# Optimization experiments

Hardware: AMD Instinct MI355X
Metric: run time of the kernel (lower is better)

## Reference

```python
import jax, jax.numpy as jnp
import numpy as np

B, T, F_IN, N, H = 16, 2048, 64, 24, 64  # batch, time, input_dim, num_nodes, hidden_dim
ALPHA = 0.2        # LeakyReLU negative slope
NEG_INF = -9e15    # mask value used by the torch module


def setup_inputs() -> dict:
    key = jax.random.key(0)
    k0, k1, k2, k3, k4 = jax.random.split(key, 5)
    x = jax.random.normal(k0, (B, T, F_IN), dtype=jnp.float32)
    adj = jax.random.randint(k1, (N, N), 0, 2, dtype=jnp.int32)  # binary adjacency
    # input_projector: Linear(input_dim, num_nodes*hidden_dim)
    Wp = jax.random.normal(k2, (F_IN, N * H), dtype=jnp.float32) * 0.05
    bp = jnp.zeros((N * H,), dtype=jnp.float32)
    # GraphAttentionLayer params: W (in=H, out=H), a (2H, 1)
    W = jax.random.normal(k3, (H, H), dtype=jnp.float32) * 0.05
    a = jax.random.normal(k4, (2 * H, 1), dtype=jnp.float32) * 0.05
    return {"x": x, "adj": adj, "Wp": Wp, "bp": bp, "W": W, "a": a}


def reference(x, adj, Wp, bp, W, a):
    Bx, Tx, Fx = x.shape
    BT = Bx * Tx
    # input projector -> per-node features (BT, N, H)
    h = (x.reshape(BT, Fx) @ Wp + bp).reshape(BT, N, H)
    # GAT layer (concat=True), eval mode so dropout is identity
    Wh = h @ W  # (BT, N, H)
    # e[b,i,j] = LeakyReLU([Wh_i ; Wh_j] @ a) = LeakyReLU(Wh_i@a1 + Wh_j@a2)
    a1, a2 = a[:H, 0], a[H:, 0]
    f1 = Wh @ a1  # (BT, N)
    f2 = Wh @ a2  # (BT, N)
    e = f1[:, :, None] + f2[:, None, :]
    e = jnp.where(e > 0, e, ALPHA * e)
    e = jnp.where(adj[None, :, :] > 0, e, jnp.float32(NEG_INF))
    attn = jax.nn.softmax(e, axis=2)  # (BT, N, N)
    h_prime = jnp.einsum('bij,bjh->bih', attn, Wh)  # (BT, N, H)
    h_prime = jax.nn.elu(h_prime)
    out = h_prime.mean(axis=1)  # mean over nodes -> (BT, H)
    return out.reshape(Bx, Tx, H)
```

## Files before the change

kernel.cpp:

```cpp
#include <hip/hip_runtime.h>
#include <hip/hip_bf16.h>

#define F_IN   64
#define NN     24
#define HH     64
#define CC     1536
#define CCX    1584
#define NTILE  99
#define ROWS   16
#define BT_TOT (16 * 2048)
#define ALPHA_ 0.2f
#define NEG_INF_ -9.0e15f
#define LOG2E_ 1.4426950408889634f
#define XSP    72
#define ATS    24

typedef short bf16x8 __attribute__((ext_vector_type(8)));
typedef float f32x4  __attribute__((ext_vector_type(4)));

#if defined(__has_builtin)
#  if __has_builtin(__builtin_amdgcn_cvt_pk_bf16_f32)
#    define HAS_PK_BF16 1
#  endif
#  if __has_builtin(__builtin_amdgcn_exp2f)
#    define HAS_EXP2 1
#  endif
#  if __has_builtin(__builtin_amdgcn_rcpf)
#    define HAS_RCP 1
#  endif
#  if __has_builtin(__builtin_amdgcn_fmed3f)
#    define HAS_MED3 1
#  endif
#endif
#ifndef HAS_PK_BF16
#  define HAS_PK_BF16 0
#endif
#ifndef HAS_EXP2
#  define HAS_EXP2 0
#endif
#ifndef HAS_RCP
#  define HAS_RCP 0
#endif
#ifndef HAS_MED3
#  define HAS_MED3 0
#endif

__device__ __forceinline__ short f2bf(float f) {
    unsigned u = __float_as_uint(f);
    return (short)((u + 0x7FFFu + ((u >> 16) & 1u)) >> 16);
}

__device__ __forceinline__ int pk2bf(float a, float b) {
#if HAS_PK_BF16
    typedef __bf16 bfv2 __attribute__((ext_vector_type(2)));
    bfv2 r = __builtin_amdgcn_cvt_pk_bf16_f32(a, b);
    return __builtin_bit_cast(int, r);
#else
    return (int)(unsigned short)f2bf(a) | ((int)f2bf(b) << 16);
#endif
}

__device__ __forceinline__ float exp2_fast(float x) {
#if HAS_EXP2
    return __builtin_amdgcn_exp2f(x);
#else
    return __expf(0.6931471805599453f * x);
#endif
}

__device__ __forceinline__ float rcp_fast(float x) {
#if HAS_RCP
    return __builtin_amdgcn_rcpf(x);
#else
    return 1.0f / x;
#endif
}

__device__ __forceinline__ float elu_fast(float v) {
#if HAS_MED3
    return __builtin_amdgcn_fmed3f(v, exp2_fast(v * LOG2E_) - 1.f, 0.f);
#else
    return (v > 0.f) ? v : (exp2_fast(v * LOG2E_) - 1.f);
#endif
}

__global__ __launch_bounds__(256) void precompute_kernel(
    const float* __restrict__ Wp,
    const float* __restrict__ bp,
    const float* __restrict__ W,
    const float* __restrict__ a,
    const int*   __restrict__ adj,
    short* __restrict__ Bpk,
    float* __restrict__ bpWx,
    float* __restrict__ maskf)
{
    __shared__ float WpS[64 * 65];
    __shared__ float WS[64 * 17];
    __shared__ float Wa[128];
    const int b = blockIdx.x, tid = threadIdx.x;

    if (b < 96) {
        const int n64 = (b >> 2) * 64;
        const int jc0 = (b & 3) * 16;
        for (int i = tid; i < 4096; i += 256)
            WpS[(i >> 6) * 65 + (i & 63)] = Wp[(size_t)(i >> 6) * CC + n64 + (i & 63)];
        for (int i = tid; i < 1024; i += 256)
            WS[(i >> 4) * 17 + (i & 15)] = W[(i >> 4) * 64 + jc0 + (i & 15)];
        __syncthreads();

        const int k = tid & 63, q0 = (tid >> 6) * 4;
        float acc[4] = {0.f, 0.f, 0.f, 0.f};
        #pragma unroll 4
        for (int m = 0; m < 64; ++m) {
            const float wp = WpS[k * 65 + m];
            #pragma unroll
            for (int j = 0; j < 4; ++j)
                acc[j] += wp * WS[m * 17 + q0 + j];
        }
        const int s2 = k >> 5, jj = k & 7, lbase = ((k >> 3) & 3) * 16;
        #pragma unroll
        for (int j = 0; j < 4; ++j) {
            const int l = lbase + q0 + j;
            Bpk[((size_t)(b * 2 + s2) * 64 + l) * 8 + jj] = f2bf(acc[j]);
        }
    } else {
        const bool needWa = (b < 108) || (b == 114);
        if (needWa) {
            if (tid < 128) {
                const int which = tid >> 6, m = tid & 63;
                float s = 0.f;
                #pragma unroll 8
                for (int h = 0; h < 64; ++h)
                    s += W[m * 64 + h] * a[which * 64 + h];
                Wa[tid] = s;
            }
            __syncthreads();
        }
        if (b < 108) {
            const int u  = (b - 96) * 256 + tid;
            const int jj = u & 7, l = (u >> 3) & 63, s2 = (u >> 9) & 1, te = u >> 10;
            const int t  = 96 + te;
            const int k  = s2 * 32 + ((l >> 4) << 3) + jj;
            const int ff = te * 16 + (l & 15);
            const int which = (ff >= NN) ? 1 : 0;
            const int node  = ff - which * NN;
            float v = 0.f;
            #pragma unroll 8
            for (int m = 0; m < 64; ++m)
                v += Wp[(size_t)k * CC + node * 64 + m] * Wa[which * 64 + m];
            Bpk[((size_t)(t * 2 + s2) * 64 + l) * 8 + jj] = f2bf(v * LOG2E_);
        } else {
            const int c = (b - 108) * 256 + tid;
            if (c < CC) {
                const int n = c >> 6, jc = c & 63;
                float s = 0.f;
                #pragma unroll 8
                for (int m = 0; m < 64; ++m) s += bp[n * 64 + m] * W[m * 64 + jc];
                bpWx[c] = s;
            } else if (c < CCX) {
                const int ff = c - CC;
                const int which = (ff >= NN) ? 1 : 0;
                const int node  = ff - which * NN;
                float s = 0.f;
                #pragma unroll 8
                for (int m = 0; m < 64; ++m) s += bp[node * 64 + m] * Wa[which * 64 + m];
                bpWx[c] = s * LOG2E_;
            }
            if (b == 114) {
                for (int i = tid; i < NN * NN; i += 256)
                    maskf[i] = (adj[i] > 0) ? 0.f : NEG_INF_;
            }
        }
    }
}

__global__ __launch_bounds__(1024, 8) void gat_main_kernel(
    const float* __restrict__ x,
    const float* __restrict__ maskf,
    const short* __restrict__ Bpk,
    const float* __restrict__ bpWx,
    float* __restrict__ out)
{
    __shared__ __align__(16) short xs16[ROWS * XSP];
    __shared__ __align__(16) short whB[ROWS * 4 * 48 * 8];
    __shared__ __align__(16) short attn16[ROWS * NN * ATS];
    __shared__ __align__(16) short zero16[8];
    __shared__ __align__(16) float maskQ[6 * 24 * 4];
    __shared__ float fs[ROWS * 48];

    const int tid  = threadIdx.x;
    const int lane = tid & 63;
    const int wid  = tid >> 6;
    const int quad = lane >> 4;
    const int lm   = lane & 15;
    const size_t base = (size_t)blockIdx.x * ROWS;

    const float xval = x[base * F_IN + tid];

    const int g  = wid >> 2;
    const int nt = wid & 3;
    bf16x8 pb0[2], pb1[2];
    float  pbias[2];
    if (wid < 12) {
        #pragma unroll
        for (int k = 0; k < 2; ++k) {
            const int t = (g * 8 + k) * 4 + nt;
            const short* bq = Bpk + ((size_t)(t * 2) * 64 + lane) * 8;
            pb0[k] = *(const bf16x8*)bq;
            pb1[k] = *(const bf16x8*)(bq + 512);
            pbias[k] = bpWx[t * 16 + lm];
        }
    } else if (wid < 15) {
        const int t = 96 + (wid - 12);
        const short* bq = Bpk + ((size_t)(t * 2) * 64 + lane) * 8;
        pb0[0] = *(const bf16x8*)bq;
        pb1[0] = *(const bf16x8*)(bq + 512);
        pbias[0] = bpWx[t * 16 + lm];
    }

    if (tid < 8) zero16[tid] = 0;
    if (tid < NN * NN) {
        const int i = tid / NN, rem = tid - i * NN;
        const int gg = (rem >= 12) ? 1 : 0;
        const int jl = rem - gg * 12;
        const int q = jl >> 2, c = jl & 3;
        maskQ[((gg * 3 + q) * NN + i) * 4 + c] = maskf[tid];
    }
    {
        const int rr = tid >> 6, k = tid & 63;
        xs16[rr * XSP + k] = f2bf(xval);
    }
    __syncthreads();

    {
        const bf16x8 a0 = *(const bf16x8*)(xs16 + lm * XSP + quad * 8);
        const bf16x8 a1 = *(const bf16x8*)(xs16 + lm * XSP + 32 + quad * 8);

        if (wid < 12) {
            short* wb0 = whB + ((nt * 48 + g * 16 + lm) * 8) + quad * 4 * 1536;
            int pA[4], pB[4];
            {
                f32x4 acc[4];
                #pragma unroll
                for (int k = 0; k < 4; ++k) {
                    bf16x8 b0, b1;
                    float bb;
                    if (k < 2) {
                        b0 = pb0[k]; b1 = pb1[k]; bb = pbias[k];
                    } else {
                        const int t = (g * 8 + k) * 4 + nt;
                        const short* bq = Bpk + ((size_t)(t * 2) * 64 + lane) * 8;
                        b0 = *(const bf16x8*)bq;
                        b1 = *(const bf16x8*)(bq + 512);
                        bb = bpWx[t * 16 + lm];
                    }
                    f32x4 c = {bb, bb, bb, bb};
                    c = __builtin_amdgcn_mfma_f32_16x16x32_bf16(a0, b0, c, 0, 0, 0);
                    c = __builtin_amdgcn_mfma_f32_16x16x32_bf16(a1, b1, c, 0, 0, 0);
                    acc[k] = c;
                }
                #pragma unroll
                for (int i = 0; i < 4; ++i) {
                    pA[i] = pk2bf(acc[0][i], acc[1][i]);
                    pB[i] = pk2bf(acc[2][i], acc[3][i]);
                }
            }
            {
                f32x4 acc[4];
                #pragma unroll
                for (int k = 0; k < 4; ++k) {
                    const int t = (g * 8 + 4 + k) * 4 + nt;
                    const short* bq = Bpk + ((size_t)(t * 2) * 64 + lane) * 8;
                    const bf16x8 b0 = *(const bf16x8*)bq;
                    const bf16x8 b1 = *(const bf16x8*)(bq + 512);
                    const float bb = bpWx[t * 16 + lm];
                    f32x4 c = {bb, bb, bb, bb};
                    c = __builtin_amdgcn_mfma_f32_16x16x32_bf16(a0, b0, c, 0, 0, 0);
                    c = __builtin_amdgcn_mfma_f32_16x16x32_bf16(a1, b1, c, 0, 0, 0);
                    acc[k] = c;
                }
                #pragma unroll
                for (int i = 0; i < 4; ++i) {
                    int4 w;
                    w.x = pA[i];
                    w.y = pB[i];
                    w.z = pk2bf(acc[0][i], acc[1][i]);
                    w.w = pk2bf(acc[2][i], acc[3][i]);
                    *(int4*)(wb0 + i * 1536) = w;
                }
            }
        } else if (wid < 15) {
            const int t = 96 + (wid - 12);
            const float bb = pbias[0];
            f32x4 acc = {bb, bb, bb, bb};
            acc = __builtin_amdgcn_mfma_f32_16x16x32_bf16(a0, pb0[0], acc, 0, 0, 0);
            acc = __builtin_amdgcn_mfma_f32_16x16x32_bf16(a1, pb1[0], acc, 0, 0, 0);
            const int ff = (t - 96) * 16 + lm;
            #pragma unroll
            for (int i = 0; i < 4; ++i)
                fs[(quad * 4 + i) * 48 + ff] = acc[i];
        }
    }
    __syncthreads();

    const int r = wid;
    short* attn_r = attn16 + r * NN * ATS;

    const int gg = lane >> 5;
    const int i  = lane & 31;
    const int jb = gg * 12;

    const float f1i = fs[r * 48 + i];
    const int mr = (i < NN) ? i : 0;

    float f2v[12], mrow[12];
    {
        const float* fp = fs + r * 48 + NN + jb;
        const float4 fa = *(const float4*)(fp);
        const float4 fb = *(const float4*)(fp + 4);
        const float4 fc = *(const float4*)(fp + 8);
        f2v[0]=fa.x; f2v[1]=fa.y; f2v[2]=fa.z; f2v[3]=fa.w;
        f2v[4]=fb.x; f2v[5]=fb.y; f2v[6]=fb.z; f2v[7]=fb.w;
        f2v[8]=fc.x; f2v[9]=fc.y; f2v[10]=fc.z; f2v[11]=fc.w;
        const float* mp = maskQ + gg * 288 + mr * 4;
        const float4 ma = *(const float4*)(mp);
        const float4 mb = *(const float4*)(mp + 96);
        const float4 mc = *(const float4*)(mp + 192);
        mrow[0]=ma.x; mrow[1]=ma.y; mrow[2]=ma.z; mrow[3]=ma.w;
        mrow[4]=mb.x; mrow[5]=mb.y; mrow[6]=mb.z; mrow[7]=mb.w;
        mrow[8]=mc.x; mrow[9]=mc.y; mrow[10]=mc.z; mrow[11]=mc.w;
    }

    float ev[12];
    float ssum = 0.f;
    #pragma unroll
    for (int j = 0; j < 12; ++j) {
        float e = f1i + f2v[j];
        e = fmaxf(e, ALPHA_ * e);
        const float p = exp2_fast(e + mrow[j]);
        ev[j] = p;
        ssum += p;
    }
    const float tot = ssum + __shfl_xor(ssum, 32, 64);
    const float inv = rcp_fast(tot);

    if (i < NN) {
        int pq[6];
        #pragma unroll
        for (int q = 0; q < 6; ++q)
            pq[q] = pk2bf(ev[2 * q] * inv, ev[2 * q + 1] * inv);
        short* dst = attn_r + i * ATS + jb;
        if (gg == 0) {
            *(int4*)(dst)     = make_int4(pq[0], pq[1], pq[2], pq[3]);
            *(int2*)(dst + 8) = make_int2(pq[4], pq[5]);
        } else {
            *(int2*)(dst)     = make_int2(pq[0], pq[1]);
            *(int4*)(dst + 4) = make_int4(pq[2], pq[3], pq[4], pq[5]);
        }
    }

    const short* pa0src = (quad < 3) ? (attn_r + lm * ATS + quad * 8) : zero16;
    const short* pa1src = (quad < 3 && lm < 8)
        ? (attn_r + (16 + lm) * ATS + quad * 8) : zero16;
    const bf16x8 pa0 = *(const bf16x8*)pa0src;
    const bf16x8 pa1 = *(const bf16x8*)pa1src;
    #pragma unroll
    for (int ntp = 0; ntp < 4; ++ntp) {
        const short* bsrc = (lane < 48)
            ? (whB + r * 1536 + (ntp * 48 + lane) * 8) : zero16;
        const bf16x8 bw = *(const bf16x8*)bsrc;
        f32x4 c0 = {0.f, 0.f, 0.f, 0.f};
        f32x4 c1 = {0.f, 0.f, 0.f, 0.f};
        __builtin_amdgcn_s_setprio(1);
        c0 = __builtin_amdgcn_mfma_f32_16x16x32_bf16(pa0, bw, c0, 0, 0, 0);
        c1 = __builtin_amdgcn_mfma_f32_16x16x32_bf16(pa1, bw, c1, 0, 0, 0);
        __builtin_amdgcn_s_setprio(0);
        float s = 0.f;
        #pragma unroll
        for (int k = 0; k < 4; ++k)
            s += elu_fast(c0[k]);
        #pragma unroll
        for (int k = 0; k < 4; ++k)
            s += elu_fast(c1[k]);
        s += __shfl_xor(s, 16, 64);
        s += __shfl_xor(s, 32, 64);
        if (quad == 0)
            out[(base + r) * HH + ntp * 16 + lm] = s * (1.0f / 24.0f);
    }
}

extern "C" void kernel_launch(void* const* d_in, const int* in_sizes, int n_in,
                              void* d_out, int out_size, void* d_ws, size_t ws_size,
                              hipStream_t stream)
{
    const float* x   = (const float*)d_in[0];
    const int*   adj = (const int*)d_in[1];
    const float* Wp  = (const float*)d_in[2];
    const float* bp  = (const float*)d_in[3];
    const float* W   = (const float*)d_in[4];
    const float* a   = (const float*)d_in[5];
    float* out = (float*)d_out;

    short* Bpk   = (short*)d_ws;
    float* bpWx  = (float*)(Bpk + (size_t)NTILE * 1024);
    float* maskf = bpWx + CCX;

    precompute_kernel<<<115, 256, 0, stream>>>(Wp, bp, W, a, adj, Bpk, bpWx, maskf);
    gat_main_kernel<<<BT_TOT / ROWS, 1024, 0, stream>>>(x, maskf, Bpk, bpWx, out);
}
```

Before: 109.3 us.

## Make main kernel persistent over eight row groups with register-resident weights

Each block now walks eight 16-row groups in a loop instead of handling one group, so the grid is eight times smaller. Half of the projection weight fragments and biases stay in registers across iterations, and the next x row is prefetched while the current group computes. This amortises per-block setup (mask reorder, weight loads) and hides x load latency. In exchange it uses more registers (launch bounds lowered to 4), adds an extra barrier per iteration, and leaves fewer blocks to spread across CUs.

Result: slower. 120.0 us (+9.8%).

```diff
diff --git a/kernel.cpp b/kernel.cpp
--- a/kernel.cpp
+++ b/kernel.cpp
@@ -8,6 +8,7 @@
 #define CCX    1584
 #define NTILE  99
 #define ROWS   16
+#define GRPS   8
 #define BT_TOT (16 * 2048)
 #define ALPHA_ 0.2f
 #define NEG_INF_ -9.0e15f
@@ -174,7 +175,7 @@
     }
 }
 
-__global__ __launch_bounds__(1024, 8) void gat_main_kernel(
+__global__ __launch_bounds__(1024, 4) void gat_main_kernel(
     const float* __restrict__ x,
     const float* __restrict__ maskf,
     const short* __restrict__ Bpk,
@@ -193,30 +194,9 @@
     const int wid  = tid >> 6;
     const int quad = lane >> 4;
     const int lm   = lane & 15;
-    const size_t base = (size_t)blockIdx.x * ROWS;
-
-    const float xval = x[base * F_IN + tid];
 
     const int g  = wid >> 2;
     const int nt = wid & 3;
-    bf16x8 pb0[2], pb1[2];
-    float  pbias[2];
-    if (wid < 12) {
-        #pragma unroll
-        for (int k = 0; k < 2; ++k) {
-            const int t = (g * 8 + k) * 4 + nt;
-            const short* bq = Bpk + ((size_t)(t * 2) * 64 + lane) * 8;
-            pb0[k] = *(const bf16x8*)bq;
-            pb1[k] = *(const bf16x8*)(bq + 512);
-            pbias[k] = bpWx[t * 16 + lm];
-        }
-    } else if (wid < 15) {
-        const int t = 96 + (wid - 12);
-        const short* bq = Bpk + ((size_t)(t * 2) * 64 + lane) * 8;
-        pb0[0] = *(const bf16x8*)bq;
-        pb1[0] = *(const bf16x8*)(bq + 512);
-        pbias[0] = bpWx[t * 16 + lm];
-    }
 
     if (tid < 8) zero16[tid] = 0;
     if (tid < NN * NN) {
@@ -226,166 +206,195 @@
         const int q = jl >> 2, c = jl & 3;
         maskQ[((gg * 3 + q) * NN + i) * 4 + c] = maskf[tid];
     }
-    {
-        const int rr = tid >> 6, k = tid & 63;
-        xs16[rr * XSP + k] = f2bf(xval);
+
+    bf16x8 rb0[4], rb1[4];
+    float  rbias[4];
+    if (wid < 12) {
+        #pragma unroll
+        for (int k = 0; k < 4; ++k) {
+            const int t = (g * 8 + k) * 4 + nt;
+            const short* bq = Bpk + ((size_t)(t * 2) * 64 + lane) * 8;
+            rb0[k] = *(const bf16x8*)bq;
+            rb1[k] = *(const bf16x8*)(bq + 512);
+            rbias[k] = bpWx[t * 16 + lm];
+        }
+    } else if (wid < 15) {
+        const int t = 96 + (wid - 12);
+        const short* bq = Bpk + ((size_t)(t * 2) * 64 + lane) * 8;
+        rb0[0] = *(const bf16x8*)bq;
+        rb1[0] = *(const bf16x8*)(bq + 512);
+        rbias[0] = bpWx[t * 16 + lm];
     }
-    __syncthreads();
-
-    {
-        const bf16x8 a0 = *(const bf16x8*)(xs16 + lm * XSP + quad * 8);
-        const bf16x8 a1 = *(const bf16x8*)(xs16 + lm * XSP + 32 + quad * 8);
-
-        if (wid < 12) {
-            short* wb0 = whB + ((nt * 48 + g * 16 + lm) * 8) + quad * 4 * 1536;
-            int pA[4], pB[4];
-            {
-                f32x4 acc[4];
+
+    const short* sbq = (wid < 12)
+        ? (Bpk + ((size_t)(((g * 8 + 4) * 4 + nt) * 2) * 64 + lane) * 8)
+        : Bpk;
+    const float* sbias = (wid < 12) ? (bpWx + ((g * 8 + 4) * 4 + nt) * 16 + lm)
+                                    : bpWx;
+
+    const size_t xstep = (size_t)ROWS * F_IN;
+    size_t xoff = (size_t)blockIdx.x * GRPS * xstep + tid;
+    float xval = x[xoff];
+
+    #pragma unroll 1
+    for (int it = 0; it < GRPS; ++it) {
+        const size_t base = (size_t)(blockIdx.x * GRPS + it) * ROWS;
+
+        {
+            const int rr = tid >> 6, k = tid & 63;
+            xs16[rr * XSP + k] = f2bf(xval);
+        }
+        __syncthreads();
+
+        if (it + 1 < GRPS) {
+            xoff += xstep;
+            xval = x[xoff];
+        }
+
+        {
+            const bf16x8 a0 = *(const bf16x8*)(xs16 + lm * XSP + quad * 8);
+            const bf16x8 a1 = *(const bf16x8*)(xs16 + lm * XSP + 32 + quad * 8);
+
+            if (wid < 12) {
+                short* wb0 = whB + ((nt * 48 + g * 16 + lm) * 8) + quad * 4 * 1536;
+                int pA[4], pB[4];
+                {
+                    f32x4 acc[4];
+                    #pragma unroll
+                    for (int k = 0; k < 4; ++k) {
+                        f32x4 c = {rbias[k], rbias[k], rbias[k], rbias[k]};
+                        c = __builtin_amdgcn_mfma_f32_16x16x32_bf16(a0, rb0[k], c, 0, 0, 0);
+                        c = __builtin_amdgcn_mfma_f32_16x16x32_bf16(a1, rb1[k], c, 0, 0, 0);
+                        acc[k] = c;
+                    }
+                    #pragma unroll
+                    for (int i = 0; i < 4; ++i) {
+                        pA[i] = pk2bf(acc[0][i], acc[1][i]);
+                        pB[i] = pk2bf(acc[2][i], acc[3][i]);
+                    }
+                }
+                {
+                    f32x4 acc[4];
+                    #pragma unroll
+                    for (int k = 0; k < 4; ++k) {
+                        const short* bq = sbq + (size_t)k * 4 * 1024;
+                        const bf16x8 b0 = *(const bf16x8*)bq;
+                        const bf16x8 b1 = *(const bf16x8*)(bq + 512);
+                        const float bb = sbias[k * 64];
+                        f32x4 c = {bb, bb, bb, bb};
+                        c = __builtin_amdgcn_mfma_f32_16x16x32_bf16(a0, b0, c, 0, 0, 0);
+                        c = __builtin_amdgcn_mfma_f32_16x16x32_bf16(a1, b1, c, 0, 0, 0);
+                        acc[k] = c;
+                    }
+                    #pragma unroll
+                    for (int i = 0; i < 4; ++i) {
+                        int4 w;
+                        w.x = pA[i];
+                        w.y = pB[i];
+                        w.z = pk2bf(acc[0][i], acc[1][i]);
+                        w.w = pk2bf(acc[2][i], acc[3][i]);
+                        *(int4*)(wb0 + i * 1536) = w;
+                    }
+                }
+            } else if (wid < 15) {
+                const int t = 96 + (wid - 12);
+                const float bb = rbias[0];
+                f32x4 acc = {bb, bb, bb, bb};
+                acc = __builtin_amdgcn_mfma_f32_16x16x32_bf16(a0, rb0[0], acc, 0, 0, 0);
+                acc = __builtin_amdgcn_mfma_f32_16x16x32_bf16(a1, rb1[0], acc, 0, 0, 0);
+                const int ff = (t - 96) * 16 + lm;
                 #pragma unroll
-                for (int k = 0; k < 4; ++k) {
-                    bf16x8 b0, b1;
-                    float bb;
-                    if (k < 2) {
-                        b0 = pb0[k]; b1 = pb1[k]; bb = pbias[k];
-                    } else {
-                        const int t = (g * 8 + k) * 4 + nt;
-                        const short* bq = Bpk + ((size_t)(t * 2) * 64 + lane) * 8;
-                        b0 = *(const bf16x8*)bq;
-                        b1 = *(const bf16x8*)(bq + 512);
-                        bb = bpWx[t * 16 + lm];
-                    }
-                    f32x4 c = {bb, bb, bb, bb};
-                    c = __builtin_amdgcn_mfma_f32_16x16x32_bf16(a0, b0, c, 0, 0, 0);
-                    c = __builtin_amdgcn_mfma_f32_16x16x32_bf16(a1, b1, c, 0, 0, 0);
-                    acc[k] = c;
-                }
-                #pragma unroll
-                for (int i = 0; i < 4; ++i) {
-                    pA[i] = pk2bf(acc[0][i], acc[1][i]);
-                    pB[i] = pk2bf(acc[2][i], acc[3][i]);
-                }
+                for (int i = 0; i < 4; ++i)
+                    fs[(quad * 4 + i) * 48 + ff] = acc[i];
             }
-            {
-                f32x4 acc[4];
-                #pragma unroll
-                for (int k = 0; k < 4; ++k) {
-                    const int t = (g * 8 + 4 + k) * 4 + nt;
-                    const short* bq = Bpk + ((size_t)(t * 2) * 64 + lane) * 8;
-                    const bf16x8 b0 = *(const bf16x8*)bq;
-                    const bf16x8 b1 = *(const bf16x8*)(bq + 512);
-                    const float bb = bpWx[t * 16 + lm];
-                    f32x4 c = {bb, bb, bb, bb};
-                    c = __builtin_amdgcn_mfma_f32_16x16x32_bf16(a0, b0, c, 0, 0, 0);
-                    c = __builtin_amdgcn_mfma_f32_16x16x32_bf16(a1, b1, c, 0, 0, 0);
-                    acc[k] = c;
-                }
-                #pragma unroll
-                for (int i = 0; i < 4; ++i) {
-                    int4 w;
-                    w.x = pA[i];
-                    w.y = pB[i];
-                    w.z = pk2bf(acc[0][i], acc[1][i]);
-                    w.w = pk2bf(acc[2][i], acc[3][i]);
-                    *(int4*)(wb0 + i * 1536) = w;
-                }
+        }
+        __syncthreads();
+
+        const int r = wid;
+        short* attn_r = attn16 + r * NN * ATS;
+
+        const int gg = lane >> 5;
+        const int i  = lane & 31;
+        const int jb = gg * 12;
+
+        const float f1i = fs[r * 48 + i];
+        const int mr = (i < NN) ? i : 0;
+
+        float f2v[12], mrow[12];
+        {
+            const float* fp = fs + r * 48 + NN + jb;
+            const float4 fa = *(const float4*)(fp);
+            const float4 fb = *(const float4*)(fp + 4);
+            const float4 fc = *(const float4*)(fp + 8);
+            f2v[0]=fa.x; f2v[1]=fa.y; f2v[2]=fa.z; f2v[3]=fa.w;
+            f2v[4]=fb.x; f2v[5]=fb.y; f2v[6]=fb.z; f2v[7]=fb.w;
+            f2v[8]=fc.x; f2v[9]=fc.y; f2v[10]=fc.z; f2v[11]=fc.w;
+            const float* mp = maskQ + gg * 288 + mr * 4;
+            const float4 ma = *(const float4*)(mp);
+            const float4 mb = *(const float4*)(mp + 96);
+            const float4 mc = *(const float4*)(mp + 192);
+            mrow[0]=ma.x; mrow[1]=ma.y; mrow[2]=ma.z; mrow[3]=ma.w;
+            mrow[4]=mb.x; mrow[5]=mb.y; mrow[6]=mb.z; mrow[7]=mb.w;
+            mrow[8]=mc.x; mrow[9]=mc.y; mrow[10]=mc.z; mrow[11]=mc.w;
+        }
+
+        float ev[12];
+        float ssum = 0.f;
+        #pragma unroll
+        for (int j = 0; j < 12; ++j) {
+            float e = f1i + f2v[j];
+            e = fmaxf(e, ALPHA_ * e);
+            const float p = exp2_fast(e + mrow[j]);
+            ev[j] = p;
+            ssum += p;
+        }
+        const float tot = ssum + __shfl_xor(ssum, 32, 64);
+        const float inv = rcp_fast(tot);
+
+        if (i < NN) {
+            int pq[6];
+            #pragma unroll
+            for (int q = 0; q < 6; ++q)
+                pq[q] = pk2bf(ev[2 * q] * inv, ev[2 * q + 1] * inv);
+            short* dst = attn_r + i * ATS + jb;
+            if (gg == 0) {
+                *(int4*)(dst)     = make_int4(pq[0], pq[1], pq[2], pq[3]);
+                *(int2*)(dst + 8) = make_int2(pq[4], pq[5]);
+            } else {
+                *(int2*)(dst)     = make_int2(pq[0], pq[1]);
+                *(int4*)(dst + 4) = make_int4(pq[2], pq[3], pq[4], pq[5]);
             }
-        } else if (wid < 15) {
-            const int t = 96 + (wid - 12);
-            const float bb = pbias[0];
-            f32x4 acc = {bb, bb, bb, bb};
-            acc = __builtin_amdgcn_mfma_f32_16x16x32_bf16(a0, pb0[0], acc, 0, 0, 0);
-            acc = __builtin_amdgcn_mfma_f32_16x16x32_bf16(a1, pb1[0], acc, 0, 0, 0);
-            const int ff = (t - 96) * 16 + lm;
+        }
+
+        const short* pa0src = (quad < 3) ? (attn_r + lm * ATS + quad * 8) : zero16;
+        const short* pa1src = (quad < 3 && lm < 8)
+            ? (attn_r + (16 + lm) * ATS + quad * 8) : zero16;
+        const bf16x8 pa0 = *(const bf16x8*)pa0src;
+        const bf16x8 pa1 = *(const bf16x8*)pa1src;
+        #pragma unroll
+        for (int ntp = 0; ntp < 4; ++ntp) {
+            const short* bsrc = (lane < 48)
+                ? (whB + r * 1536 + (ntp * 48 + lane) * 8) : zero16;
+            const bf16x8 bw = *(const bf16x8*)bsrc;
+            f32x4 c0 = {0.f, 0.f, 0.f, 0.f};
+            f32x4 c1 = {0.f, 0.f, 0.f, 0.f};
+            __builtin_amdgcn_s_setprio(1);
+            c0 = __builtin_amdgcn_mfma_f32_16x16x32_bf16(pa0, bw, c0, 0, 0, 0);
+            c1 = __builtin_amdgcn_mfma_f32_16x16x32_bf16(pa1, bw, c1, 0, 0, 0);
+            __builtin_amdgcn_s_setprio(0);
+            float s = 0.f;
             #pragma unroll
-            for (int i = 0; i < 4; ++i)
-                fs[(quad * 4 + i) * 48 + ff] = acc[i];
-        }
-    }
-    __syncthreads();
-
-    const int r = wid;
-    short* attn_r = attn16 + r * NN * ATS;
-
-    const int gg = lane >> 5;
-    const int i  = lane & 31;
-    const int jb = gg * 12;
-
-    const float f1i = fs[r * 48 + i];
-    const int mr = (i < NN) ? i : 0;
-
-    float f2v[12], mrow[12];
-    {
-        const float* fp = fs + r * 48 + NN + jb;
-        const float4 fa = *(const float4*)(fp);
-        const float4 fb = *(const float4*)(fp + 4);
-        const float4 fc = *(const float4*)(fp + 8);
-        f2v[0]=fa.x; f2v[1]=fa.y; f2v[2]=fa.z; f2v[3]=fa.w;
-        f2v[4]=fb.x; f2v[5]=fb.y; f2v[6]=fb.z; f2v[7]=fb.w;
-        f2v[8]=fc.x; f2v[9]=fc.y; f2v[10]=fc.z; f2v[11]=fc.w;
-        const float* mp = maskQ + gg * 288 + mr * 4;
-        const float4 ma = *(const float4*)(mp);
-        const float4 mb = *(const float4*)(mp + 96);
-        const float4 mc = *(const float4*)(mp + 192);
-        mrow[0]=ma.x; mrow[1]=ma.y; mrow[2]=ma.z; mrow[3]=ma.w;
-        mrow[4]=mb.x; mrow[5]=mb.y; mrow[6]=mb.z; mrow[7]=mb.w;
-        mrow[8]=mc.x; mrow[9]=mc.y; mrow[10]=mc.z; mrow[11]=mc.w;
-    }
-
-    float ev[12];
-    float ssum = 0.f;
-    #pragma unroll
-    for (int j = 0; j < 12; ++j) {
-        float e = f1i + f2v[j];
-        e = fmaxf(e, ALPHA_ * e);
-        const float p = exp2_fast(e + mrow[j]);
-        ev[j] = p;
-        ssum += p;
-    }
-    const float tot = ssum + __shfl_xor(ssum, 32, 64);
-    const float inv = rcp_fast(tot);
-
-    if (i < NN) {
-        int pq[6];
-        #pragma unroll
-        for (int q = 0; q < 6; ++q)
-            pq[q] = pk2bf(ev[2 * q] * inv, ev[2 * q + 1] * inv);
-        short* dst = attn_r + i * ATS + jb;
-        if (gg == 0) {
-            *(int4*)(dst)     = make_int4(pq[0], pq[1], pq[2], pq[3]);
-            *(int2*)(dst + 8) = make_int2(pq[4], pq[5]);
-        } else {
-            *(int2*)(dst)     = make_int2(pq[0], pq[1]);
-            *(int4*)(dst + 4) = make_int4(pq[2], pq[3], pq[4], pq[5]);
-        }
-    }
-
-    const short* pa0src = (quad < 3) ? (attn_r + lm * ATS + quad * 8) : zero16;
-    const short* pa1src = (quad < 3 && lm < 8)
-        ? (attn_r + (16 + lm) * ATS + quad * 8) : zero16;
-    const bf16x8 pa0 = *(const bf16x8*)pa0src;
-    const bf16x8 pa1 = *(const bf16x8*)pa1src;
-    #pragma unroll
-    for (int ntp = 0; ntp < 4; ++ntp) {
-        const short* bsrc = (lane < 48)
-            ? (whB + r * 1536 + (ntp * 48 + lane) * 8) : zero16;
-        const bf16x8 bw = *(const bf16x8*)bsrc;
-        f32x4 c0 = {0.f, 0.f, 0.f, 0.f};
-        f32x4 c1 = {0.f, 0.f, 0.f, 0.f};
-        __builtin_amdgcn_s_setprio(1);
-        c0 = __builtin_amdgcn_mfma_f32_16x16x32_bf16(pa0, bw, c0, 0, 0, 0);
-        c1 = __builtin_amdgcn_mfma_f32_16x16x32_bf16(pa1, bw, c1, 0, 0, 0);
-        __builtin_amdgcn_s_setprio(0);
-        float s = 0.f;
-        #pragma unroll
-        for (int k = 0; k < 4; ++k)
-            s += elu_fast(c0[k]);
-        #pragma unroll
-        for (int k = 0; k < 4; ++k)
-            s += elu_fast(c1[k]);
-        s += __shfl_xor(s, 16, 64);
-        s += __shfl_xor(s, 32, 64);
-        if (quad == 0)
-            out[(base + r) * HH + ntp * 16 + lm] = s * (1.0f / 24.0f);
+            for (int k = 0; k < 4; ++k)
+                s += elu_fast(c0[k]);
+            #pragma unroll
+            for (int k = 0; k < 4; ++k)
+                s += elu_fast(c1[k]);
+            s += __shfl_xor(s, 16, 64);
+            s += __shfl_xor(s, 32, 64);
+            if (quad == 0)
+                out[(base + r) * HH + ntp * 16 + lm] = s * (1.0f / 24.0f);
+        }
+        __syncthreads();
     }
 }
 
@@ -406,5 +415,5 @@
     float* maskf = bpWx + CCX;
 
     precompute_kernel<<<115, 256, 0, stream>>>(Wp, bp, W, a, adj, Bpk, bpWx, maskf);
-    gat_main_kernel<<<BT_TOT / ROWS, 1024, 0, stream>>>(x, maskf, Bpk, bpWx, out);
-}
+    gat_main_kernel<<<BT_TOT / (ROWS * GRPS), 1024, 0, stream>>>(x, maskf, Bpk, bpWx, out);
+}
```
